# Performance work log

Measured on AMD Instinct MI355X. Metric: run time of the kernel, lower is better.

Reference implementation:

```python
import jax, jax.numpy as jnp
import numpy as np

SPATIAL_SHAPES = [(80, 80), (40, 40), (20, 20), (10, 10)]
NUM_POINTS = [4, 4, 4, 4]
N_HEADS = 8
D_MODEL = 256
OFFSET_SCALE = 0.5


def setup_inputs() -> dict:
    key = jax.random.key(0)
    ks = jax.random.split(key, 7)
    bs, Lq = 32, 300
    Lv = sum(h * w for h, w in SPATIAL_SHAPES)  # 8500
    tp = N_HEADS * sum(NUM_POINTS)  # 128
    return {
        'query': jax.random.normal(ks[0], (bs, Lq, D_MODEL), jnp.float32),
        'reference_points': jax.random.uniform(ks[1], (bs, Lq, 1, 4), jnp.float32),
        'value': jax.random.normal(ks[2], (bs, Lv, D_MODEL), jnp.float32),
        'w_off': 0.02 * jax.random.normal(ks[3], (D_MODEL, tp * 2), jnp.float32),
        'b_off': 0.1 * jax.random.normal(ks[4], (tp * 2,), jnp.float32),
        'w_attn': 0.02 * jax.random.normal(ks[5], (D_MODEL, tp), jnp.float32),
        'b_attn': 0.02 * jax.random.normal(ks[6], (tp,), jnp.float32),
    }


def _bilinear_sample(v, grid):
    # v: [B, c, h, w]; grid: [B, Q, P, 2] in [-1, 1]
    # F.grid_sample(mode='bilinear', padding_mode='zeros', align_corners=False)
    B, c, h, w = v.shape
    x = (grid[..., 0] + 1.0) * (w * 0.5) - 0.5
    y = (grid[..., 1] + 1.0) * (h * 0.5) - 0.5
    x0 = jnp.floor(x)
    y0 = jnp.floor(y)
    wx1 = x - x0
    wy1 = y - y0
    x0i = x0.astype(jnp.int32)
    y0i = y0.astype(jnp.int32)
    vflat = v.reshape(B, c, h * w)

    def gather(xi, yi):
        valid = ((xi >= 0) & (xi < w) & (yi >= 0) & (yi < h)).astype(v.dtype)
        idx = jnp.clip(yi, 0, h - 1) * w + jnp.clip(xi, 0, w - 1)
        g = jnp.take_along_axis(vflat, idx.reshape(B, 1, -1), axis=2)
        return g.reshape(B, c, *xi.shape[1:]) * valid[:, None]

    out = (gather(x0i, y0i) * ((1.0 - wx1) * (1.0 - wy1))[:, None]
           + gather(x0i + 1, y0i) * (wx1 * (1.0 - wy1))[:, None]
           + gather(x0i, y0i + 1) * ((1.0 - wx1) * wy1)[:, None]
           + gather(x0i + 1, y0i + 1) * (wx1 * wy1)[:, None])
    return out  # [B, c, Q, P]


def reference(query, reference_points, value, w_off, b_off, w_attn, b_attn):
    bs, Lq, _ = query.shape
    H = N_HEADS
    c = D_MODEL // H
    sumP = sum(NUM_POINTS)

    # sampling offsets and attention weights from the query
    off = (query @ w_off + b_off).reshape(bs, Lq, H, sumP, 2)
    attn = jax.nn.softmax((query @ w_attn + b_attn).reshape(bs, Lq, H, sumP), axis=-1)

    # reference_points last dim == 4 path (box cx,cy,w,h)
    nps = jnp.asarray([1.0 / n for n in NUM_POINTS for _ in range(n)], query.dtype)[:, None]  # [sumP,1]
    loc = (reference_points[:, :, None, :, :2]
           + off * nps * reference_points[:, :, None, :, 2:] * OFFSET_SCALE)  # [bs,Lq,H,sumP,2]

    grids = (2.0 * loc - 1.0).transpose(0, 2, 1, 3, 4).reshape(bs * H, Lq, sumP, 2)

    # value [bs, Lv, C] -> per-head feature maps [bs*H, c, Lv]
    v = value.reshape(bs, -1, H, c).transpose(0, 2, 3, 1).reshape(bs * H, c, -1)

    sampled = []
    start = 0
    pstart = 0
    for (h, w), p in zip(SPATIAL_SHAPES, NUM_POINTS):
        v_l = v[:, :, start:start + h * w].reshape(bs * H, c, h, w)
        g_l = grids[:, :, pstart:pstart + p]  # [bs*H, Lq, p, 2]
        sampled.append(_bilinear_sample(v_l, g_l))  # [bs*H, c, Lq, p]
        start += h * w
        pstart += p
    sampled = jnp.concatenate(sampled, axis=-1)  # [bs*H, c, Lq, sumP]

    aw = attn.transpose(0, 2, 1, 3).reshape(bs * H, 1, Lq, sumP)
    out = (sampled * aw).sum(-1)  # [bs*H, c, Lq]
    return out.reshape(bs, H * c, Lq).transpose(0, 2, 1)  # [bs, Lq, C]
```

## Files before the change

### kernel.cpp

```cpp
#include <hip/hip_runtime.h>
#include <math.h>

#define BS     32
#define LQ     300
#define DM     256
#define NH     8
#define CH     32
#define SUMP   16
#define LV     8500
#define MROWS  (BS*LQ)
#define NW     384

__global__ __launch_bounds__(256) void gemm_off_attn(
    const float* __restrict__ A,
    const float* __restrict__ Boff,
    const float* __restrict__ Batt,
    const float* __restrict__ bias_off,
    const float* __restrict__ bias_att,
    float* __restrict__ C)
{
    __shared__ float As[32][68];
    __shared__ float Bs[32][68];

    const int tid = threadIdx.x;
    const int m0  = blockIdx.x * 64;
    const int n0  = blockIdx.y * 64;

    const float* Bp; int ldb, nb0; const float* biasp;
    if (n0 < 256) { Bp = Boff; ldb = 256; nb0 = n0;       biasp = bias_off + n0; }
    else          { Bp = Batt; ldb = 128; nb0 = n0 - 256; biasp = bias_att + (n0 - 256); }

    const int tx = tid & 15;
    const int ty = tid >> 4;

    const int am = tid >> 3;
    const int ak = (tid & 7) * 4;
    const int bk = tid >> 4;
    const int bn = (tid & 15) * 4;

    float acc[4][4] = {};

    for (int k0 = 0; k0 < 256; k0 += 32) {
        #pragma unroll
        for (int pp = 0; pp < 2; ++pp) {
            const int m = pp * 32 + am;
            float4 a = *(const float4*)&A[(size_t)(m0 + m) * DM + k0 + ak];
            As[ak + 0][m] = a.x; As[ak + 1][m] = a.y;
            As[ak + 2][m] = a.z; As[ak + 3][m] = a.w;
            const int k = pp * 16 + bk;
            float4 b = *(const float4*)&Bp[(size_t)(k0 + k) * ldb + nb0 + bn];
            *(float4*)&Bs[k][bn] = b;
        }
        __syncthreads();
        #pragma unroll
        for (int k = 0; k < 32; ++k) {
            float4 av = *(const float4*)&As[k][ty * 4];
            float4 bv = *(const float4*)&Bs[k][tx * 4];
            float a[4] = {av.x, av.y, av.z, av.w};
            float b[4] = {bv.x, bv.y, bv.z, bv.w};
            #pragma unroll
            for (int i = 0; i < 4; ++i)
                #pragma unroll
                for (int j = 0; j < 4; ++j)
                    acc[i][j] = fmaf(a[i], b[j], acc[i][j]);
        }
        __syncthreads();
    }

    float4 bias = *(const float4*)&biasp[tx * 4];
    const float bb[4] = {bias.x, bias.y, bias.z, bias.w};
    #pragma unroll
    for (int i = 0; i < 4; ++i) {
        const int m = m0 + ty * 4 + i;
        float4 o;
        o.x = acc[i][0] + bb[0]; o.y = acc[i][1] + bb[1];
        o.z = acc[i][2] + bb[2]; o.w = acc[i][3] + bb[3];
        *(float4*)&C[(size_t)m * NW + n0 + tx * 4] = o;
    }
}

__global__ __launch_bounds__(256) void ms_deform(
    const float* __restrict__ P,
    const float* __restrict__ ref,
    const float* __restrict__ value,
    float* __restrict__ out)
{
    const int lane = threadIdx.x & 31;
    const int gid  = blockIdx.x * 8 + (threadIdx.x >> 5);
    const int h    = gid & 7;
    const int bq   = gid >> 3;
    const int b    = bq / LQ;

    const float4 r    = *(const float4*)&ref[(size_t)bq * 4];
    const float* prow = P + (size_t)bq * NW;

    float w[SUMP];
    float mx = -1e30f;
    #pragma unroll
    for (int p = 0; p < SUMP; ++p) {
        w[p] = prow[256 + h * SUMP + p];
        mx = fmaxf(mx, w[p]);
    }
    float ssum = 0.f;
    #pragma unroll
    for (int p = 0; p < SUMP; ++p) { w[p] = __expf(w[p] - mx); ssum += w[p]; }
    const float inv = 1.f / ssum;

    const int Wd[4] = {80, 40, 20, 10};
    const int St[4] = {0, 6400, 8000, 8400};

    const float* vb0 = value + (size_t)b * LV * DM + h * CH + lane;
    float acc = 0.f;

    #pragma unroll
    for (int p = 0; p < SUMP; ++p) {
        const int lvl = p >> 2;
        const int W   = Wd[lvl];
        const float* vb = vb0 + (size_t)St[lvl] * DM;

        const float ox = prow[(h * SUMP + p) * 2 + 0];
        const float oy = prow[(h * SUMP + p) * 2 + 1];
        const float x = (r.x + ox * r.z * 0.125f) * (float)W - 0.5f;
        const float y = (r.y + oy * r.w * 0.125f) * (float)W - 0.5f;

        const float xf = floorf(x), yf = floorf(y);
        const float fx = x - xf,    fy = y - yf;
        const int   ix = (int)xf,   iy = (int)yf;

        const bool xv0 = (ix >= 0)     & (ix < W);
        const bool xv1 = (ix + 1 >= 0) & (ix + 1 < W);
        const bool yv0 = (iy >= 0)     & (iy < W);
        const bool yv1 = (iy + 1 >= 0) & (iy + 1 < W);

        const int cell = iy * W + ix;
        float v00 = 0.f, v10 = 0.f, v01 = 0.f, v11 = 0.f;
        if (xv0 & yv0) v00 = vb[(size_t)((cell)         ) * DM];
        if (xv1 & yv0) v10 = vb[(size_t)((cell + 1)     ) * DM];
        if (xv0 & yv1) v01 = vb[(size_t)((cell + W)     ) * DM];
        if (xv1 & yv1) v11 = vb[(size_t)((cell + W + 1) ) * DM];

        const float sv = (1.f - fx) * (1.f - fy) * v00 + fx * (1.f - fy) * v10
                       + (1.f - fx) * fy         * v01 + fx * fy         * v11;
        acc = fmaf(w[p], sv, acc);
    }

    out[(size_t)bq * DM + h * CH + lane] = acc * inv;
}

extern "C" void kernel_launch(void* const* d_in, const int* in_sizes, int n_in,
                              void* d_out, int out_size, void* d_ws, size_t ws_size,
                              hipStream_t stream) {
    const float* query  = (const float*)d_in[0];
    const float* refpts = (const float*)d_in[1];
    const float* value  = (const float*)d_in[2];
    const float* w_off  = (const float*)d_in[3];
    const float* b_off  = (const float*)d_in[4];
    const float* w_attn = (const float*)d_in[5];
    const float* b_attn = (const float*)d_in[6];
    float* out = (float*)d_out;
    float* P   = (float*)d_ws;

    dim3 gg(MROWS / 64, NW / 64);
    gemm_off_attn<<<gg, 256, 0, stream>>>(query, w_off, w_attn, b_off, b_attn, P);

    ms_deform<<<(BS * LQ * NH) / 8, 256, 0, stream>>>(P, refpts, value, out);
}
```

Baseline: 494.5 us.

## Remap deformable sampling to full 64-lane wavefronts with float4 corner gathers

Measured after the change: 418.3 us. 1.18x faster.

```diff
diff --git a/kernel.cpp b/kernel.cpp
--- a/kernel.cpp
+++ b/kernel.cpp
@@ -85,66 +85,100 @@
     const float* __restrict__ value,
     float* __restrict__ out)
 {
-    const int lane = threadIdx.x & 31;
-    const int gid  = blockIdx.x * 8 + (threadIdx.x >> 5);
+    const int tid  = threadIdx.x;
+    const int lane = tid & 63;
+    const int gid  = blockIdx.x * 4 + (tid >> 6);
     const int h    = gid & 7;
     const int bq   = gid >> 3;
     const int b    = bq / LQ;
 
+    const int p2     = lane >> 5;
+    const int corner = (lane >> 3) & 3;
+    const int c4     = lane & 7;
+
     const float4 r    = *(const float4*)&ref[(size_t)bq * 4];
     const float* prow = P + (size_t)bq * NW;
 
-    float w[SUMP];
+    float4 o[8];
+    #pragma unroll
+    for (int k = 0; k < 8; ++k) o[k] = *(const float4*)&prow[h * 32 + k * 4];
+
+    float4 L[4];
+    #pragma unroll
+    for (int k = 0; k < 4; ++k) L[k] = *(const float4*)&prow[256 + h * 16 + k * 4];
+
     float mx = -1e30f;
     #pragma unroll
-    for (int p = 0; p < SUMP; ++p) {
-        w[p] = prow[256 + h * SUMP + p];
-        mx = fmaxf(mx, w[p]);
-    }
+    for (int k = 0; k < 4; ++k)
+        mx = fmaxf(mx, fmaxf(fmaxf(L[k].x, L[k].y), fmaxf(L[k].z, L[k].w)));
     float ssum = 0.f;
     #pragma unroll
-    for (int p = 0; p < SUMP; ++p) { w[p] = __expf(w[p] - mx); ssum += w[p]; }
+    for (int k = 0; k < 4; ++k) {
+        L[k].x = __expf(L[k].x - mx); ssum += L[k].x;
+        L[k].y = __expf(L[k].y - mx); ssum += L[k].y;
+        L[k].z = __expf(L[k].z - mx); ssum += L[k].z;
+        L[k].w = __expf(L[k].w - mx); ssum += L[k].w;
+    }
     const float inv = 1.f / ssum;
+
+    const float* vb0 = value + (size_t)b * LV * DM + h * CH + c4 * 4;
 
     const int Wd[4] = {80, 40, 20, 10};
     const int St[4] = {0, 6400, 8000, 8400};
 
-    const float* vb0 = value + (size_t)b * LV * DM + h * CH + lane;
-    float acc = 0.f;
-
-    #pragma unroll
-    for (int p = 0; p < SUMP; ++p) {
-        const int lvl = p >> 2;
+    float4 acc = {0.f, 0.f, 0.f, 0.f};
+
+    #pragma unroll
+    for (int it = 0; it < 8; ++it) {
+        const int lvl = it >> 1;
         const int W   = Wd[lvl];
-        const float* vb = vb0 + (size_t)St[lvl] * DM;
-
-        const float ox = prow[(h * SUMP + p) * 2 + 0];
-        const float oy = prow[(h * SUMP + p) * 2 + 1];
-        const float x = (r.x + ox * r.z * 0.125f) * (float)W - 0.5f;
-        const float y = (r.y + oy * r.w * 0.125f) * (float)W - 0.5f;
-
+        const float fW = (float)W;
+
+        const float ox = p2 ? o[it].z : o[it].x;
+        const float oy = p2 ? o[it].w : o[it].y;
+
+        float wA, wB;
+        if ((it & 1) == 0) { wA = L[lvl].x; wB = L[lvl].y; }
+        else               { wA = L[lvl].z; wB = L[lvl].w; }
+        const float wp = p2 ? wB : wA;
+
+        const float x = (r.x + ox * r.z * 0.125f) * fW - 0.5f;
+        const float y = (r.y + oy * r.w * 0.125f) * fW - 0.5f;
         const float xf = floorf(x), yf = floorf(y);
         const float fx = x - xf,    fy = y - yf;
-        const int   ix = (int)xf,   iy = (int)yf;
-
-        const bool xv0 = (ix >= 0)     & (ix < W);
-        const bool xv1 = (ix + 1 >= 0) & (ix + 1 < W);
-        const bool yv0 = (iy >= 0)     & (iy < W);
-        const bool yv1 = (iy + 1 >= 0) & (iy + 1 < W);
-
-        const int cell = iy * W + ix;
-        float v00 = 0.f, v10 = 0.f, v01 = 0.f, v11 = 0.f;
-        if (xv0 & yv0) v00 = vb[(size_t)((cell)         ) * DM];
-        if (xv1 & yv0) v10 = vb[(size_t)((cell + 1)     ) * DM];
-        if (xv0 & yv1) v01 = vb[(size_t)((cell + W)     ) * DM];
-        if (xv1 & yv1) v11 = vb[(size_t)((cell + W + 1) ) * DM];
-
-        const float sv = (1.f - fx) * (1.f - fy) * v00 + fx * (1.f - fy) * v10
-                       + (1.f - fx) * fy         * v01 + fx * fy         * v11;
-        acc = fmaf(w[p], sv, acc);
-    }
-
-    out[(size_t)bq * DM + h * CH + lane] = acc * inv;
+
+        const int ix = (int)xf + (corner & 1);
+        const int iy = (int)yf + ((corner >> 1) & 1);
+        const bool valid = (ix >= 0) & (ix < W) & (iy >= 0) & (iy < W);
+        const int ixc = min(max(ix, 0), W - 1);
+        const int iyc = min(max(iy, 0), W - 1);
+
+        const float4 v = *(const float4*)&vb0[(size_t)(St[lvl] + iyc * W + ixc) * DM];
+
+        const float wx = (corner & 1) ? fx : 1.f - fx;
+        const float wy = (corner & 2) ? fy : 1.f - fy;
+        const float s  = wp * wx * wy * (valid ? 1.f : 0.f);
+
+        acc.x = fmaf(s, v.x, acc.x);
+        acc.y = fmaf(s, v.y, acc.y);
+        acc.z = fmaf(s, v.z, acc.z);
+        acc.w = fmaf(s, v.w, acc.w);
+    }
+
+    #pragma unroll
+    for (int m = 8; m <= 32; m <<= 1) {
+        acc.x += __shfl_xor(acc.x, m, 64);
+        acc.y += __shfl_xor(acc.y, m, 64);
+        acc.z += __shfl_xor(acc.z, m, 64);
+        acc.w += __shfl_xor(acc.w, m, 64);
+    }
+
+    if (lane < 8) {
+        float4 ov;
+        ov.x = acc.x * inv; ov.y = acc.y * inv;
+        ov.z = acc.z * inv; ov.w = acc.w * inv;
+        *(float4*)&out[(size_t)bq * DM + h * CH + c4 * 4] = ov;
+    }
 }
 
 extern "C" void kernel_launch(void* const* d_in, const int* in_sizes, int n_in,
@@ -163,5 +197,5 @@
     dim3 gg(MROWS / 64, NW / 64);
     gemm_off_attn<<<gg, 256, 0, stream>>>(query, w_off, w_attn, b_off, b_attn, P);
 
-    ms_deform<<<(BS * LQ * NH) / 8, 256, 0, stream>>>(P, refpts, value, out);
+    ms_deform<<<(BS * LQ * NH) / 4, 256, 0, stream>>>(P, refpts, value, out);
 }
```

## Restructure deformable sampling: per-query block, precomputed corner weights, float4 gathers

Applied to the files above, without the earlier changes.

After: 396.3 us. 19.8% less time.

```diff
diff --git a/kernel.cpp b/kernel.cpp
--- a/kernel.cpp
+++ b/kernel.cpp
@@ -85,66 +85,106 @@
     const float* __restrict__ value,
     float* __restrict__ out)
 {
-    const int lane = threadIdx.x & 31;
-    const int gid  = blockIdx.x * 8 + (threadIdx.x >> 5);
-    const int h    = gid & 7;
-    const int bq   = gid >> 3;
-    const int b    = bq / LQ;
-
-    const float4 r    = *(const float4*)&ref[(size_t)bq * 4];
-    const float* prow = P + (size_t)bq * NW;
-
-    float w[SUMP];
-    float mx = -1e30f;
-    #pragma unroll
-    for (int p = 0; p < SUMP; ++p) {
-        w[p] = prow[256 + h * SUMP + p];
-        mx = fmaxf(mx, w[p]);
-    }
-    float ssum = 0.f;
-    #pragma unroll
-    for (int p = 0; p < SUMP; ++p) { w[p] = __expf(w[p] - mx); ssum += w[p]; }
-    const float inv = 1.f / ssum;
+    __shared__ float  s_P[384];
+    __shared__ float4 s_ref;
+    __shared__ float  s_data[128][8];
+
+    const int bid = blockIdx.x;
+    const int bq  = (bid & 7) * 1200 + (bid >> 3);
+    const int tid = threadIdx.x;
+    const int b   = bq / LQ;
+
+    if (tid < 96) ((float4*)s_P)[tid] = ((const float4*)(P + (size_t)bq * NW))[tid];
+    if (tid == 96) s_ref = *(const float4*)&ref[(size_t)bq * 4];
+    __syncthreads();
 
     const int Wd[4] = {80, 40, 20, 10};
     const int St[4] = {0, 6400, 8000, 8400};
 
-    const float* vb0 = value + (size_t)b * LV * DM + h * CH + lane;
-    float acc = 0.f;
-
-    #pragma unroll
-    for (int p = 0; p < SUMP; ++p) {
-        const int lvl = p >> 2;
-        const int W   = Wd[lvl];
-        const float* vb = vb0 + (size_t)St[lvl] * DM;
-
-        const float ox = prow[(h * SUMP + p) * 2 + 0];
-        const float oy = prow[(h * SUMP + p) * 2 + 1];
-        const float x = (r.x + ox * r.z * 0.125f) * (float)W - 0.5f;
-        const float y = (r.y + oy * r.w * 0.125f) * (float)W - 0.5f;
-
+    if (tid < 128) {
+        const int h = tid >> 4, p = tid & 15, lvl = p >> 2;
+        const float4 r = s_ref;
+        const float lg = s_P[256 + h * 16 + p];
+        float m = lg;
+        #pragma unroll
+        for (int mk = 1; mk <= 8; mk <<= 1) m = fmaxf(m, __shfl_xor(m, mk, 64));
+        const float e = __expf(lg - m);
+        float s = e;
+        #pragma unroll
+        for (int mk = 1; mk <= 8; mk <<= 1) s += __shfl_xor(s, mk, 64);
+        const float wn = e / s;
+
+        const float ox = s_P[h * 32 + p * 2], oy = s_P[h * 32 + p * 2 + 1];
+        const int   W  = Wd[lvl];
+        const float fW = (float)W;
+        const float x  = (r.x + ox * r.z * 0.125f) * fW - 0.5f;
+        const float y  = (r.y + oy * r.w * 0.125f) * fW - 0.5f;
         const float xf = floorf(x), yf = floorf(y);
         const float fx = x - xf,    fy = y - yf;
-        const int   ix = (int)xf,   iy = (int)yf;
-
-        const bool xv0 = (ix >= 0)     & (ix < W);
-        const bool xv1 = (ix + 1 >= 0) & (ix + 1 < W);
-        const bool yv0 = (iy >= 0)     & (iy < W);
-        const bool yv1 = (iy + 1 >= 0) & (iy + 1 < W);
-
-        const int cell = iy * W + ix;
-        float v00 = 0.f, v10 = 0.f, v01 = 0.f, v11 = 0.f;
-        if (xv0 & yv0) v00 = vb[(size_t)((cell)         ) * DM];
-        if (xv1 & yv0) v10 = vb[(size_t)((cell + 1)     ) * DM];
-        if (xv0 & yv1) v01 = vb[(size_t)((cell + W)     ) * DM];
-        if (xv1 & yv1) v11 = vb[(size_t)((cell + W + 1) ) * DM];
-
-        const float sv = (1.f - fx) * (1.f - fy) * v00 + fx * (1.f - fy) * v10
-                       + (1.f - fx) * fy         * v01 + fx * fy         * v11;
-        acc = fmaf(w[p], sv, acc);
-    }
-
-    out[(size_t)bq * DM + h * CH + lane] = acc * inv;
+        const int ix0 = (int)xf, iy0 = (int)yf;
+        const float xv0 = (ix0 >= 0     && ix0 < W)     ? 1.f : 0.f;
+        const float xv1 = (ix0 + 1 >= 0 && ix0 + 1 < W) ? 1.f : 0.f;
+        const float yv0 = (iy0 >= 0     && iy0 < W)     ? 1.f : 0.f;
+        const float yv1 = (iy0 + 1 >= 0 && iy0 + 1 < W) ? 1.f : 0.f;
+        s_data[tid][0] = wn * (1.f - fx) * (1.f - fy) * xv0 * yv0;
+        s_data[tid][1] = wn * fx         * (1.f - fy) * xv1 * yv0;
+        s_data[tid][2] = wn * (1.f - fx) * fy         * xv0 * yv1;
+        s_data[tid][3] = wn * fx         * fy         * xv1 * yv1;
+        s_data[tid][4] = __int_as_float(ix0);
+        s_data[tid][5] = __int_as_float(iy0);
+    }
+    __syncthreads();
+
+    const int w    = tid >> 6;
+    const int lane = tid & 63;
+    const int grp  = lane >> 3;
+    const int c4   = lane & 7;
+
+    const float* vbase = value + (size_t)b * LV * DM + c4 * 4;
+
+    float4 accA = {0.f, 0.f, 0.f, 0.f};
+    float4 accB = {0.f, 0.f, 0.f, 0.f};
+
+    #pragma unroll
+    for (int i = 0; i < 16; ++i) {
+        const int g      = w * 128 + i * 8 + grp;
+        const int corner = g & 3;
+        const int hp     = g >> 2;
+        const int p      = hp & 15;
+        const int h      = g >> 6;
+        const int lvl    = p >> 2;
+        const int W      = Wd[lvl];
+
+        const float wc = s_data[hp][corner];
+        int ix = __float_as_int(s_data[hp][4]) + (corner & 1);
+        int iy = __float_as_int(s_data[hp][5]) + (corner >> 1);
+        ix = min(max(ix, 0), W - 1);
+        iy = min(max(iy, 0), W - 1);
+        const size_t flat = (size_t)(St[lvl] + iy * W + ix);
+
+        const float4 v = *(const float4*)&vbase[flat * DM + h * CH];
+
+        if (i < 8) {
+            accA.x = fmaf(wc, v.x, accA.x); accA.y = fmaf(wc, v.y, accA.y);
+            accA.z = fmaf(wc, v.z, accA.z); accA.w = fmaf(wc, v.w, accA.w);
+        } else {
+            accB.x = fmaf(wc, v.x, accB.x); accB.y = fmaf(wc, v.y, accB.y);
+            accB.z = fmaf(wc, v.z, accB.z); accB.w = fmaf(wc, v.w, accB.w);
+        }
+    }
+
+    #pragma unroll
+    for (int mk = 8; mk <= 32; mk <<= 1) {
+        accA.x += __shfl_xor(accA.x, mk, 64); accA.y += __shfl_xor(accA.y, mk, 64);
+        accA.z += __shfl_xor(accA.z, mk, 64); accA.w += __shfl_xor(accA.w, mk, 64);
+        accB.x += __shfl_xor(accB.x, mk, 64); accB.y += __shfl_xor(accB.y, mk, 64);
+        accB.z += __shfl_xor(accB.z, mk, 64); accB.w += __shfl_xor(accB.w, mk, 64);
+    }
+
+    if (lane < 8) {
+        *(float4*)&out[(size_t)bq * DM + (2 * w)     * CH + c4 * 4] = accA;
+        *(float4*)&out[(size_t)bq * DM + (2 * w + 1) * CH + c4 * 4] = accB;
+    }
 }
 
 extern "C" void kernel_launch(void* const* d_in, const int* in_sizes, int n_in,
@@ -163,5 +203,5 @@
     dim3 gg(MROWS / 64, NW / 64);
     gemm_off_attn<<<gg, 256, 0, stream>>>(query, w_off, w_attn, b_off, b_attn, P);
 
-    ms_deform<<<(BS * LQ * NH) / 8, 256, 0, stream>>>(P, refpts, value, out);
+    ms_deform<<<MROWS, 256, 0, stream>>>(P, refpts, value, out);
 }
```
